# Kernel optimization log

Measured on AMD Instinct MI355X. Metric: run time of the kernel, lower is better.

Reference implementation:

```python
import jax, jax.numpy as jnp
import numpy as np

H, D, KD, E = 8, 128, 16, 128
B, G = 16, 501

def setup_inputs() -> dict:
    key = jax.random.key(0)
    ks = jax.random.split(key, 12)
    stdv = 1.0 / np.sqrt(KD)
    u = lambda k, shape, s: jax.random.uniform(k, shape, jnp.float32, -s, s)
    inp = {"q": jax.random.normal(ks[0], (B, G, D), jnp.float32)}
    names = ["W_query", "W_key", "W_val", "W1_query", "W2_query", "W3_query",
             "W4_query", "W5_query", "W6_query"]
    for i, n in enumerate(names):
        inp[n] = u(ks[i + 1], (H, D, KD), stdv)
    inp["W_out"] = u(ks[10], (H, KD, E), 1.0 / np.sqrt(E))
    return inp

def _forward(q, W_query, W_key, W_val, W1, W2, W3, W4, W5, W6, W_out):
    h = q  # self-attention: h defaults to q
    b, g, d = h.shape
    np_ = (g - 1) // 2
    norm = 1.0 / jnp.sqrt(jnp.float32(KD))
    pick = h[:, 1:np_ + 1]          # [b, np, d]
    delivery = h[:, np_ + 1:]       # [b, np, d]
    proj = lambda x, W: jnp.einsum('bnd,hdk->hbnk', x, W)
    Q = proj(q, W_query); K = proj(h, W_key); V = proj(h, W_val)
    K_pick = proj(pick, W_key); V_pick = proj(pick, W_val)
    K_del = proj(delivery, W_key); V_del = proj(delivery, W_val)
    Q_pick = proj(pick, W1); Q_pick_ap = proj(pick, W2); Q_pick_ad = proj(pick, W3)
    Q_del = proj(delivery, W4); Q_del_ad = proj(delivery, W5); Q_del_ap = proj(delivery, W6)

    comp = norm * jnp.einsum('hbqk,hbgk->hbqg', Q, K)                 # [h,b,g,g]
    c_pd = norm * jnp.sum(Q_pick * K_del, -1)                          # [h,b,np]
    c_p_ap = norm * jnp.einsum('hbqk,hbpk->hbqp', Q_pick_ap, K_pick)   # [h,b,np,np]
    c_p_ad = norm * jnp.einsum('hbqk,hbpk->hbqp', Q_pick_ad, K_del)
    c_dp = norm * jnp.sum(Q_del * K_pick, -1)                          # [h,b,np]
    c_d_ad = norm * jnp.einsum('hbqk,hbpk->hbqp', Q_del_ad, K_del)
    c_d_ap = norm * jnp.einsum('hbqk,hbpk->hbqp', Q_del_ap, K_pick)

    ninf = lambda *s: jnp.full(s, -jnp.inf, comp.dtype)
    # pad branch scores to query length g (depot row + wrong-subset rows = -inf)
    c_add_del = jnp.concatenate([ninf(H, b, 1), c_pd, ninf(H, b, np_)], -1)[..., None]            # [h,b,g,1]
    c_add_ap = jnp.concatenate([ninf(H, b, 1, np_), c_p_ap, ninf(H, b, np_, np_)], 2)             # [h,b,g,np]
    c_add_ad = jnp.concatenate([ninf(H, b, 1, np_), c_p_ad, ninf(H, b, np_, np_)], 2)
    c_add_pick = jnp.concatenate([ninf(H, b, 1), ninf(H, b, np_), c_dp], -1)[..., None]
    c_add_ad2 = jnp.concatenate([ninf(H, b, 1, np_), ninf(H, b, np_, np_), c_d_ad], 2)
    c_add_ap2 = jnp.concatenate([ninf(H, b, 1, np_), ninf(H, b, np_, np_), c_d_ap], 2)
    comp_full = jnp.concatenate([comp, c_add_del, c_add_ap, c_add_ad,
                                 c_add_pick, c_add_ad2, c_add_ap2], -1)  # [h,b,g,g+2+4*np]

    attn = jax.nn.softmax(comp_full, axis=-1)

    z = lambda *s: jnp.zeros(s, V.dtype)
    V_add_del = jnp.concatenate([z(H, b, 1, KD), V_del, z(H, b, np_, KD)], 2)   # [h,b,g,kd]
    V_add_pick = jnp.concatenate([z(H, b, 1, KD), z(H, b, np_, KD), V_pick], 2)

    mm = lambda a, v: jnp.einsum('hbqp,hbpk->hbqk', a, v)
    heads = mm(attn[..., :g], V)
    heads = heads + attn[..., g:g + 1] * V_add_del
    heads = heads + mm(attn[..., g + 1:g + 1 + np_], V_pick)
    heads = heads + mm(attn[..., g + 1 + np_:g + 1 + 2 * np_], V_del)
    heads = heads + attn[..., g + 1 + 2 * np_:g + 2 + 2 * np_] * V_add_pick
    heads = heads + mm(attn[..., g + 2 + 2 * np_:g + 2 + 3 * np_], V_del)
    heads = heads + mm(attn[..., g + 2 + 3 * np_:], V_pick)

    return jnp.einsum('hbnk,hke->bne', heads, W_out)

def reference(q, W_query, W_key, W_val, W1_query, W2_query, W3_query,
              W4_query, W5_query, W6_query, W_out):
    return _forward(q, W_query, W_key, W_val, W1_query, W2_query, W3_query,
                    W4_query, W5_query, W6_query, W_out)
```

## Files before the change

### kernel.cpp

```cpp
#include <hip/hip_runtime.h>

#define H_ 8
#define D_ 128
#define KD_ 16
#define E_ 128
#define B_ 16
#define G_ 501
#define NP_ 250
#define BN_ (B_*G_)

typedef __bf16 bf16x8 __attribute__((ext_vector_type(8)));
typedef float f32x4 __attribute__((ext_vector_type(4)));
typedef unsigned short u16x8 __attribute__((ext_vector_type(8)));
typedef unsigned short u16x4 __attribute__((ext_vector_type(4)));
typedef bf16x8 __attribute__((may_alias)) bf16x8_a;
typedef u16x8 __attribute__((may_alias)) u16x8_a;
typedef u16x4 __attribute__((may_alias)) u16x4_a;

__device__ __forceinline__ unsigned short f2bf(float f) {
  unsigned int u = __builtin_bit_cast(unsigned int, f);
  unsigned int r = u + 0x7FFFu + ((u >> 16) & 1u);
  return (unsigned short)(r >> 16);
}
__device__ __forceinline__ float bf2f(unsigned short u) {
  unsigned int v = ((unsigned int)u) << 16;
  return __builtin_bit_cast(float, v);
}

__global__ __launch_bounds__(256) void k_prep(
    const float* __restrict__ w0, const float* __restrict__ w1, const float* __restrict__ w2,
    const float* __restrict__ w3, const float* __restrict__ w4, const float* __restrict__ w5,
    const float* __restrict__ w6, const float* __restrict__ w7, const float* __restrict__ w8,
    unsigned short* __restrict__ wct) {
  int i = blockIdx.x * 256 + threadIdx.x;
  if (i < H_*9*KD_*D_) {
    int d = i & 127; int t = i >> 7; int k = t & 15; t >>= 4;
    int wi = t % 9; int h = t / 9;
    const float* src = w0;
    switch (wi) {
      case 1: src = w1; break; case 2: src = w2; break; case 3: src = w3; break;
      case 4: src = w4; break; case 5: src = w5; break; case 6: src = w6; break;
      case 7: src = w7; break; case 8: src = w8; break; default: break;
    }
    wct[i] = f2bf(src[h*(D_*KD_) + d*KD_ + k]);
  }
}

__global__ __launch_bounds__(256) void k_proj(const float* __restrict__ q,
                                              const unsigned short* __restrict__ wct,
                                              unsigned short* __restrict__ P) {
  const int tid = threadIdx.x;
  const int lane = tid & 63;
  const int wv = tid >> 6;
  const int ln = lane & 15;
  const int quad = lane >> 4;
  const int b = blockIdx.y >> 3;
  const int nt = blockIdx.y & 7;
  const int cbase = blockIdx.x * 64;

  __shared__ __align__(16) unsigned short sA[64*136];
  __shared__ __align__(16) unsigned short sB[64*136];

  for (int i = tid; i < 1024; i += 256) {
    int rr = i >> 4, half = i & 15;
    int r = min(nt*64 + rr, G_ - 1);
    const float* src = q + (size_t)(b*G_ + r)*D_ + half*8;
    float4 f0 = ((const float4*)src)[0];
    float4 f1 = ((const float4*)src)[1];
    u16x8 v;
    v[0]=f2bf(f0.x); v[1]=f2bf(f0.y); v[2]=f2bf(f0.z); v[3]=f2bf(f0.w);
    v[4]=f2bf(f1.x); v[5]=f2bf(f1.y); v[6]=f2bf(f1.z); v[7]=f2bf(f1.w);
    *(u16x8*)(sA + rr*136 + half*8) = v;
  }
  for (int i = tid; i < 1024; i += 256) {
    int cc = i >> 4, half = i & 15;
    u16x8 v = *(const u16x8*)(wct + (size_t)(cbase + cc)*D_ + half*8);
    *(u16x8*)(sB + cc*136 + half*8) = v;
  }
  __syncthreads();

  bf16x8 a[4];
  #pragma unroll
  for (int ks = 0; ks < 4; ++ks)
    a[ks] = *(const bf16x8_a*)(sA + (wv*16 + ln)*136 + ks*32 + quad*8);

  #pragma unroll
  for (int ct = 0; ct < 4; ++ct) {
    f32x4 acc = {0.f,0.f,0.f,0.f};
    #pragma unroll
    for (int ks = 0; ks < 4; ++ks) {
      bf16x8 bb = *(const bf16x8_a*)(sB + (ct*16 + ln)*136 + ks*32 + quad*8);
      acc = __builtin_amdgcn_mfma_f32_16x16x32_bf16(a[ks], bb, acc, 0,0,0);
    }
    const int c = cbase + ct*16 + ln;
    const int h = c / 144; const int rem = c - h*144; const int w = rem >> 4; const int k = rem & 15;
    const float sc = (w == 1 || w == 2) ? 1.0f : 0.25f;
    const size_t pb = ((size_t)((h*9 + w)*B_ + b)*G_)*KD_ + k;
    #pragma unroll
    for (int g = 0; g < 4; ++g) {
      const int nn = nt*64 + wv*16 + quad*4 + g;
      if (nn < G_) P[pb + (size_t)nn*KD_] = f2bf(acc[g]*sc);
    }
  }
}

__device__ __forceinline__ f32x4 mf(bf16x8 a, bf16x8 b, f32x4 c) {
  return __builtin_amdgcn_mfma_f32_16x16x32_bf16(a, b, c, 0,0,0);
}

__device__ __forceinline__ void score_chunk(
    int c, bool up, bool dn, int cbuf,
    const unsigned short* sK, bf16x8 qa, bf16x8 qp, bf16x8 qdl,
    unsigned short* eb, float rv, float& esum, int ln, int quad)
{
  const f32x4 z4 = {0.f,0.f,0.f,0.f};
  bf16x8 k0 = {}, k1 = {};
  if (quad < 2) {
    const unsigned short* kp = sK + (c*32 + ln)*16 + quad*8;
    k0 = *(const bf16x8_a*)(kp);
    k1 = *(const bf16x8_a*)(kp + 256);
  }
  f32x4 sa0 = mf(k0, qa, z4), sa1 = mf(k1, qa, z4);
  f32x4 sp0 = z4, sp1 = z4, sd0 = z4, sd1 = z4;
  if (up) { sp0 = mf(k0, qp, z4);  sp1 = mf(k1, qp, z4); }
  if (dn) { sd0 = mf(k0, qdl, z4); sd1 = mf(k1, qdl, z4); }

  float el = 0.f;
  unsigned short ev[8];
  #pragma unroll
  for (int t = 0; t < 2; ++t) {
    #pragma unroll
    for (int rg = 0; rg < 4; ++rg) {
      float comp = __expf(t ? sa1[rg] : sa0[rg]);
      if (c == 15 && t == 1) comp *= (quad*4 + rg <= 4) ? 1.f : 0.f;
      float ex = 0.f;
      if (up) {
        float m = 1.f;
        if (c == 0 && t == 0 && rg == 0) m = (quad != 0) ? 1.f : 0.f;
        if (c == 7 && t == 1) m = (quad*4 + rg <= 10) ? 1.f : 0.f;
        ex += m * __expf(t ? sp1[rg] : sp0[rg]);
      }
      if (dn) {
        float m = 1.f;
        if (c == 7)  m = (t == 1 && quad*4 + rg >= 11) ? 1.f : 0.f;
        if (c == 15 && t == 1) m = (quad*4 + rg <= 4) ? 1.f : 0.f;
        ex += m * __expf(t ? sd1[rg] : sd0[rg]);
      }
      float e = comp + rv * ex;
      el += e;
      ev[t*4 + rg] = f2bf(e);
    }
  }
  esum += el;
  u16x4 w0, w1;
  w0[0]=ev[0]; w0[1]=ev[1]; w0[2]=ev[2]; w0[3]=ev[3];
  w1[0]=ev[4]; w1[1]=ev[5]; w1[2]=ev[6]; w1[3]=ev[7];
  unsigned short* base = eb + cbuf*640 + ln*40 + quad*4;
  *(u16x4_a*)(base)      = w0;
  *(u16x4_a*)(base + 16) = w1;
}

__global__ __launch_bounds__(256, 3) void k_attn(const unsigned short* __restrict__ P,
                                                 float* __restrict__ heads) {
  const int rt = blockIdx.x, b = blockIdx.y, h = blockIdx.z;
  const int tid = threadIdx.x;
  const int lane = tid & 63;
  const int wv = tid >> 6;
  const int ln = lane & 15;
  const int quad = lane >> 4;
  const int r0 = rt * 64;

  __shared__ __align__(16) unsigned short sK [512*16];
  __shared__ __align__(16) unsigned short sVt[16*520];
  __shared__ __align__(16) unsigned short sQa[65*16];
  __shared__ __align__(16) unsigned short sQp[65*16];
  __shared__ __align__(16) unsigned short sQd[65*16];
  __shared__ __align__(16) unsigned short sQs[65*16];
  __shared__ __align__(16) unsigned short sKs[65*16];
  __shared__ __align__(16) unsigned short eBuf[4*2*640];

  const size_t slab = (size_t)G_*KD_;
  const unsigned short* Pk = P + ((size_t)(h*9+1)*B_ + b)*slab;
  const unsigned short* Pv = P + ((size_t)(h*9+2)*B_ + b)*slab;
  const u16x8 vz = {0,0,0,0,0,0,0,0};

  for (int i = tid; i < 1024; i += 256) {
    int key = i >> 1;
    u16x8 v = vz;
    if (key < G_) v = *(const u16x8*)(Pk + key*KD_ + (i & 1)*8);
    *(u16x8*)(sK + i*8) = v;
  }
  for (int i = tid; i < 8192; i += 256) {
    int key = i >> 4, kd = i & 15;
    sVt[kd*520 + key] = (key < G_) ? Pv[key*KD_ + kd] : (unsigned short)0;
  }
  for (int i = tid; i < 650; i += 256) {
    int arr = i / 130;
    int j = i - arr*130;
    int rr = j >> 1, half = j & 1;
    int r = r0 + rr;
    u16x8 v = vz;
    if (rr < 64 && r < G_) {
      bool pick = (r <= NP_);
      const unsigned short* src;
      if (arr == 4) {
        int ks = (r == 0) ? 0 : (pick ? r + NP_ : r - NP_);
        src = Pk + ks*KD_;
      } else {
        int w = (arr == 0) ? 0 : (arr == 1) ? (pick ? 4 : 8)
              : (arr == 2) ? (pick ? 5 : 7) : (pick ? 3 : 6);
        src = P + ((size_t)(h*9 + w)*B_ + b)*slab + (size_t)r*KD_;
      }
      v = *(const u16x8*)(src + half*8);
    }
    unsigned short* dst = (arr==0) ? sQa : (arr==1) ? sQp : (arr==2) ? sQd
                        : (arr==3) ? sQs : sKs;
    *(u16x8*)(dst + j*8) = v;
  }
  __syncthreads();

  const int aoff = (wv*16 + ln)*16 + quad*8;
  bf16x8 qa  = *(const bf16x8_a*)(sQa + aoff);
  bf16x8 qp  = *(const bf16x8_a*)(sQp + aoff);
  bf16x8 qdl = *(const bf16x8_a*)(sQd + aoff);

  const int rw0 = r0 + wv*16;
  const int ra = rw0 + ln;
  const float rv = (ra >= 1) ? 1.f : 0.f;
  unsigned short* eb = eBuf + wv*1280;

  f32x4 acc = {0.f,0.f,0.f,0.f};
  float esum = 0.f;

  #pragma unroll
  for (int p = 0; p < 8; ++p) {
    const int c0 = 2*p, c1 = c0 + 1;
    score_chunk(c0, c0 <= 7, c0 >= 7, 0, sK, qa, qp, qdl, eb, rv, esum, ln, quad);
    score_chunk(c1, c1 <= 7, c1 >= 7, 1, sK, qa, qp, qdl, eb, rv, esum, ln, quad);
    #pragma unroll
    for (int u = 0; u < 2; ++u) {
      bf16x8 Ef = *(const bf16x8_a*)(eb + u*640 + ln*40 + quad*8);
      bf16x8 Vf = *(const bf16x8_a*)(sVt + ln*520 + (c0+u)*32 + quad*8);
      acc = mf(Vf, Ef, acc);
    }
  }

  esum += __shfl_xor(esum, 16);
  esum += __shfl_xor(esum, 32);

  const unsigned short* qsp = sQs + (wv*16 + ln)*16;
  const unsigned short* ksp = sKs + (wv*16 + ln)*16;
  u16x8 qs0 = *(const u16x8_a*)(qsp), qs1 = *(const u16x8_a*)(qsp + 8);
  u16x8 ks0 = *(const u16x8_a*)(ksp), ks1 = *(const u16x8_a*)(ksp + 8);
  float s = 0.f;
  #pragma unroll
  for (int kd = 0; kd < 8; ++kd) {
    s = fmaf(bf2f(qs0[kd]), bf2f(ks0[kd]), s);
    s = fmaf(bf2f(qs1[kd]), bf2f(ks1[kd]), s);
  }
  const float rvs = (ra >= 1 && ra < G_) ? 1.f : 0.f;
  const float esng = rvs * __expf(s);
  esum += esng;
  const int kpair = (ra >= 1 && ra < G_) ? ((ra <= NP_) ? ra + NP_ : ra - NP_) : 0;

  const float rcp = __builtin_amdgcn_rcpf(esum);
  float4 o;
  o.x = (acc[0] + esng * bf2f(sVt[(quad*4+0)*520 + kpair])) * rcp;
  o.y = (acc[1] + esng * bf2f(sVt[(quad*4+1)*520 + kpair])) * rcp;
  o.z = (acc[2] + esng * bf2f(sVt[(quad*4+2)*520 + kpair])) * rcp;
  o.w = (acc[3] + esng * bf2f(sVt[(quad*4+3)*520 + kpair])) * rcp;
  if (ra < G_)
    *(float4*)(heads + ((size_t)(b*G_ + ra))*E_ + h*16 + quad*4) = o;
}

__global__ __launch_bounds__(256) void k_out(const float* __restrict__ heads,
                                             const float* __restrict__ wout,
                                             float* __restrict__ out) {
  const int base = blockIdx.x * 16;
  const int tid = threadIdx.x;
  __shared__ __align__(16) float sA[16*128];
  for (int i = tid; i < 512; i += 256)
    ((float4*)sA)[i] = ((const float4*)heads)[(size_t)base*32 + i];
  __syncthreads();
  const int cg = tid & 31, rh = tid >> 5;
  float4 acc0 = make_float4(0.f,0.f,0.f,0.f);
  float4 acc1 = make_float4(0.f,0.f,0.f,0.f);
  const float4* w4 = (const float4*)wout;
  #pragma unroll 8
  for (int kk = 0; kk < 128; ++kk) {
    float4 wv = w4[kk*32 + cg];
    float a0 = sA[(rh*2)*128 + kk];
    float a1 = sA[(rh*2+1)*128 + kk];
    acc0.x = fmaf(a0, wv.x, acc0.x); acc0.y = fmaf(a0, wv.y, acc0.y);
    acc0.z = fmaf(a0, wv.z, acc0.z); acc0.w = fmaf(a0, wv.w, acc0.w);
    acc1.x = fmaf(a1, wv.x, acc1.x); acc1.y = fmaf(a1, wv.y, acc1.y);
    acc1.z = fmaf(a1, wv.z, acc1.z); acc1.w = fmaf(a1, wv.w, acc1.w);
  }
  ((float4*)out)[(size_t)(base + rh*2)*32 + cg] = acc0;
  ((float4*)out)[(size_t)(base + rh*2 + 1)*32 + cg] = acc1;
}

extern "C" void kernel_launch(void* const* d_in, const int* in_sizes, int n_in,
                              void* d_out, int out_size, void* d_ws, size_t ws_size,
                              hipStream_t stream) {
  const float* q = (const float*)d_in[0];
  const float* w0 = (const float*)d_in[1];
  const float* w1 = (const float*)d_in[2];
  const float* w2 = (const float*)d_in[3];
  const float* w3 = (const float*)d_in[4];
  const float* w4 = (const float*)d_in[5];
  const float* w5 = (const float*)d_in[6];
  const float* w6 = (const float*)d_in[7];
  const float* w7 = (const float*)d_in[8];
  const float* w8 = (const float*)d_in[9];
  const float* wout = (const float*)d_in[10];
  float* out = (float*)d_out;

  char* ws = (char*)d_ws;
  unsigned short* wct = (unsigned short*)(ws);
  unsigned short* P   = (unsigned short*)(ws + 294912);
  float* heads        = (float*)(ws + 18763776);

  k_prep<<<dim3(4608), dim3(256), 0, stream>>>(w0,w1,w2,w3,w4,w5,w6,w7,w8, wct);
  k_proj<<<dim3(18, 128), dim3(256), 0, stream>>>(q, wct, P);
  k_attn<<<dim3(8, 16, 8), dim3(256), 0, stream>>>(P, heads);
  k_out<<<dim3(501), dim3(256), 0, stream>>>(heads, wout, out);
}
```

Before: 144.0 us.

## Pre-transpose V in projection, process two row tiles per attention block, MFMA output GEMM

The projection kernel now writes V directly in a transposed, padded layout, so the attention kernel can load it with vector copies instead of a scalar transpose. Each attention block handles two 64-row query tiles, reusing the shared K/V staging. The key buffer uses a padded stride, and the single-key term reads K from shared memory. Heads are stored as bf16 and the output projection switches to a bf16 MFMA GEMM; this adds rounding error and lowers occupancy to 2 blocks per CU, while halving the attention grid.

New measurement: 123.4 us. 1.17x faster.

```diff
diff --git a/kernel.cpp b/kernel.cpp
--- a/kernel.cpp
+++ b/kernel.cpp
@@ -31,7 +31,7 @@
     const float* __restrict__ w0, const float* __restrict__ w1, const float* __restrict__ w2,
     const float* __restrict__ w3, const float* __restrict__ w4, const float* __restrict__ w5,
     const float* __restrict__ w6, const float* __restrict__ w7, const float* __restrict__ w8,
-    unsigned short* __restrict__ wct) {
+    unsigned short* __restrict__ wct, unsigned short* __restrict__ Pvt) {
   int i = blockIdx.x * 256 + threadIdx.x;
   if (i < H_*9*KD_*D_) {
     int d = i & 127; int t = i >> 7; int k = t & 15; t >>= 4;
@@ -44,11 +44,16 @@
     }
     wct[i] = f2bf(src[h*(D_*KD_) + d*KD_ + k]);
   }
+  if (i < 128*16*19) {
+    int s = i / 304; int r2 = i - s*304; int k = r2 / 19; int key = 501 + (r2 - k*19);
+    Pvt[(size_t)s*8320 + k*520 + key] = 0;
+  }
 }
 
 __global__ __launch_bounds__(256) void k_proj(const float* __restrict__ q,
                                               const unsigned short* __restrict__ wct,
-                                              unsigned short* __restrict__ P) {
+                                              unsigned short* __restrict__ P,
+                                              unsigned short* __restrict__ Pvt) {
   const int tid = threadIdx.x;
   const int lane = tid & 63;
   const int wv = tid >> 6;
@@ -94,12 +99,21 @@
     }
     const int c = cbase + ct*16 + ln;
     const int h = c / 144; const int rem = c - h*144; const int w = rem >> 4; const int k = rem & 15;
-    const float sc = (w == 1 || w == 2) ? 1.0f : 0.25f;
-    const size_t pb = ((size_t)((h*9 + w)*B_ + b)*G_)*KD_ + k;
-    #pragma unroll
-    for (int g = 0; g < 4; ++g) {
-      const int nn = nt*64 + wv*16 + quad*4 + g;
-      if (nn < G_) P[pb + (size_t)nn*KD_] = f2bf(acc[g]*sc);
+    if (w == 2) {
+      unsigned short* dstv = Pvt + (size_t)(h*B_ + b)*8320 + k*520;
+      #pragma unroll
+      for (int g = 0; g < 4; ++g) {
+        const int nn = nt*64 + wv*16 + quad*4 + g;
+        if (nn < G_) dstv[nn] = f2bf(acc[g]);
+      }
+    } else {
+      const float sc = (w == 1) ? 1.0f : 0.25f;
+      const size_t pb = ((size_t)((h*9 + w)*B_ + b)*G_)*KD_ + k;
+      #pragma unroll
+      for (int g = 0; g < 4; ++g) {
+        const int nn = nt*64 + wv*16 + quad*4 + g;
+        if (nn < G_) P[pb + (size_t)nn*KD_] = f2bf(acc[g]*sc);
+      }
     }
   }
 }
@@ -116,9 +130,9 @@
   const f32x4 z4 = {0.f,0.f,0.f,0.f};
   bf16x8 k0 = {}, k1 = {};
   if (quad < 2) {
-    const unsigned short* kp = sK + (c*32 + ln)*16 + quad*8;
+    const unsigned short* kp = sK + (c*32 + ln)*24 + quad*8;
     k0 = *(const bf16x8_a*)(kp);
-    k1 = *(const bf16x8_a*)(kp + 256);
+    k1 = *(const bf16x8_a*)(kp + 384);
   }
   f32x4 sa0 = mf(k0, qa, z4), sa1 = mf(k1, qa, z4);
   f32x4 sp0 = z4, sp1 = z4, sd0 = z4, sd1 = z4;
@@ -160,144 +174,143 @@
   *(u16x4_a*)(base + 16) = w1;
 }
 
-__global__ __launch_bounds__(256, 3) void k_attn(const unsigned short* __restrict__ P,
-                                                 float* __restrict__ heads) {
-  const int rt = blockIdx.x, b = blockIdx.y, h = blockIdx.z;
+__global__ __launch_bounds__(256, 2) void k_attn(const unsigned short* __restrict__ P,
+                                                 const unsigned short* __restrict__ Pvt,
+                                                 unsigned short* __restrict__ headsb) {
+  const int rt2 = blockIdx.x, b = blockIdx.y, h = blockIdx.z;
   const int tid = threadIdx.x;
   const int lane = tid & 63;
   const int wv = tid >> 6;
   const int ln = lane & 15;
   const int quad = lane >> 4;
-  const int r0 = rt * 64;
-
-  __shared__ __align__(16) unsigned short sK [512*16];
+
+  __shared__ __align__(16) unsigned short sK [512*24];
   __shared__ __align__(16) unsigned short sVt[16*520];
-  __shared__ __align__(16) unsigned short sQa[65*16];
-  __shared__ __align__(16) unsigned short sQp[65*16];
-  __shared__ __align__(16) unsigned short sQd[65*16];
-  __shared__ __align__(16) unsigned short sQs[65*16];
-  __shared__ __align__(16) unsigned short sKs[65*16];
+  __shared__ __align__(16) unsigned short sQ [8*1040];
   __shared__ __align__(16) unsigned short eBuf[4*2*640];
 
   const size_t slab = (size_t)G_*KD_;
   const unsigned short* Pk = P + ((size_t)(h*9+1)*B_ + b)*slab;
-  const unsigned short* Pv = P + ((size_t)(h*9+2)*B_ + b)*slab;
   const u16x8 vz = {0,0,0,0,0,0,0,0};
 
   for (int i = tid; i < 1024; i += 256) {
-    int key = i >> 1;
+    int key = i >> 1, half = i & 1;
     u16x8 v = vz;
-    if (key < G_) v = *(const u16x8*)(Pk + key*KD_ + (i & 1)*8);
-    *(u16x8*)(sK + i*8) = v;
-  }
-  for (int i = tid; i < 8192; i += 256) {
-    int key = i >> 4, kd = i & 15;
-    sVt[kd*520 + key] = (key < G_) ? Pv[key*KD_ + kd] : (unsigned short)0;
-  }
-  for (int i = tid; i < 650; i += 256) {
-    int arr = i / 130;
-    int j = i - arr*130;
+    if (key < G_) v = *(const u16x8*)(Pk + key*KD_ + half*8);
+    *(u16x8*)(sK + key*24 + half*8) = v;
+  }
+  const unsigned short* pv = Pvt + (size_t)(h*B_ + b)*8320;
+  for (int i = tid; i < 1040; i += 256)
+    *(u16x8*)(sVt + i*8) = *(const u16x8*)(pv + i*8);
+  for (int i = tid; i < 1040; i += 256) {
+    int t = i / 520; int j2 = i - t*520;
+    int arr = j2 / 130; int j = j2 - arr*130;
     int rr = j >> 1, half = j & 1;
-    int r = r0 + rr;
+    int r = (rt2*2 + t)*64 + rr;
     u16x8 v = vz;
     if (rr < 64 && r < G_) {
       bool pick = (r <= NP_);
-      const unsigned short* src;
-      if (arr == 4) {
-        int ks = (r == 0) ? 0 : (pick ? r + NP_ : r - NP_);
-        src = Pk + ks*KD_;
-      } else {
-        int w = (arr == 0) ? 0 : (arr == 1) ? (pick ? 4 : 8)
-              : (arr == 2) ? (pick ? 5 : 7) : (pick ? 3 : 6);
-        src = P + ((size_t)(h*9 + w)*B_ + b)*slab + (size_t)r*KD_;
-      }
-      v = *(const u16x8*)(src + half*8);
-    }
-    unsigned short* dst = (arr==0) ? sQa : (arr==1) ? sQp : (arr==2) ? sQd
-                        : (arr==3) ? sQs : sKs;
-    *(u16x8*)(dst + j*8) = v;
+      int w = (arr==0) ? 0 : (arr==1) ? (pick?4:8) : (arr==2) ? (pick?5:7) : (pick?3:6);
+      v = *(const u16x8*)(P + ((size_t)(h*9+w)*B_ + b)*slab + (size_t)r*KD_ + half*8);
+    }
+    *(u16x8*)(sQ + (t*4+arr)*1040 + j*8) = v;
   }
   __syncthreads();
 
-  const int aoff = (wv*16 + ln)*16 + quad*8;
-  bf16x8 qa  = *(const bf16x8_a*)(sQa + aoff);
-  bf16x8 qp  = *(const bf16x8_a*)(sQp + aoff);
-  bf16x8 qdl = *(const bf16x8_a*)(sQd + aoff);
-
-  const int rw0 = r0 + wv*16;
-  const int ra = rw0 + ln;
-  const float rv = (ra >= 1) ? 1.f : 0.f;
   unsigned short* eb = eBuf + wv*1280;
 
-  f32x4 acc = {0.f,0.f,0.f,0.f};
-  float esum = 0.f;
-
-  #pragma unroll
-  for (int p = 0; p < 8; ++p) {
-    const int c0 = 2*p, c1 = c0 + 1;
-    score_chunk(c0, c0 <= 7, c0 >= 7, 0, sK, qa, qp, qdl, eb, rv, esum, ln, quad);
-    score_chunk(c1, c1 <= 7, c1 >= 7, 1, sK, qa, qp, qdl, eb, rv, esum, ln, quad);
-    #pragma unroll
-    for (int u = 0; u < 2; ++u) {
-      bf16x8 Ef = *(const bf16x8_a*)(eb + u*640 + ln*40 + quad*8);
-      bf16x8 Vf = *(const bf16x8_a*)(sVt + ln*520 + (c0+u)*32 + quad*8);
-      acc = mf(Vf, Ef, acc);
-    }
-  }
-
-  esum += __shfl_xor(esum, 16);
-  esum += __shfl_xor(esum, 32);
-
-  const unsigned short* qsp = sQs + (wv*16 + ln)*16;
-  const unsigned short* ksp = sKs + (wv*16 + ln)*16;
-  u16x8 qs0 = *(const u16x8_a*)(qsp), qs1 = *(const u16x8_a*)(qsp + 8);
-  u16x8 ks0 = *(const u16x8_a*)(ksp), ks1 = *(const u16x8_a*)(ksp + 8);
-  float s = 0.f;
-  #pragma unroll
-  for (int kd = 0; kd < 8; ++kd) {
-    s = fmaf(bf2f(qs0[kd]), bf2f(ks0[kd]), s);
-    s = fmaf(bf2f(qs1[kd]), bf2f(ks1[kd]), s);
-  }
-  const float rvs = (ra >= 1 && ra < G_) ? 1.f : 0.f;
-  const float esng = rvs * __expf(s);
-  esum += esng;
-  const int kpair = (ra >= 1 && ra < G_) ? ((ra <= NP_) ? ra + NP_ : ra - NP_) : 0;
-
-  const float rcp = __builtin_amdgcn_rcpf(esum);
-  float4 o;
-  o.x = (acc[0] + esng * bf2f(sVt[(quad*4+0)*520 + kpair])) * rcp;
-  o.y = (acc[1] + esng * bf2f(sVt[(quad*4+1)*520 + kpair])) * rcp;
-  o.z = (acc[2] + esng * bf2f(sVt[(quad*4+2)*520 + kpair])) * rcp;
-  o.w = (acc[3] + esng * bf2f(sVt[(quad*4+3)*520 + kpair])) * rcp;
-  if (ra < G_)
-    *(float4*)(heads + ((size_t)(b*G_ + ra))*E_ + h*16 + quad*4) = o;
-}
-
-__global__ __launch_bounds__(256) void k_out(const float* __restrict__ heads,
+  for (int t = 0; t < 2; ++t) {
+    const int r0 = (rt2*2 + t)*64;
+    const unsigned short* sQt = sQ + t*4160;
+    const int aoff = (wv*16 + ln)*16 + quad*8;
+    bf16x8 qa  = *(const bf16x8_a*)(sQt + aoff);
+    bf16x8 qp  = *(const bf16x8_a*)(sQt + 1040 + aoff);
+    bf16x8 qdl = *(const bf16x8_a*)(sQt + 2080 + aoff);
+
+    const int ra = r0 + wv*16 + ln;
+    const float rv = (ra >= 1) ? 1.f : 0.f;
+
+    f32x4 acc = {0.f,0.f,0.f,0.f};
+    float esum = 0.f;
+
+    #pragma unroll
+    for (int p = 0; p < 8; ++p) {
+      const int c0 = 2*p, c1 = c0 + 1;
+      score_chunk(c0, c0 <= 7, c0 >= 7, 0, sK, qa, qp, qdl, eb, rv, esum, ln, quad);
+      score_chunk(c1, c1 <= 7, c1 >= 7, 1, sK, qa, qp, qdl, eb, rv, esum, ln, quad);
+      #pragma unroll
+      for (int u = 0; u < 2; ++u) {
+        bf16x8 Ef = *(const bf16x8_a*)(eb + u*640 + ln*40 + quad*8);
+        bf16x8 Vf = *(const bf16x8_a*)(sVt + ln*520 + (c0+u)*32 + quad*8);
+        acc = mf(Vf, Ef, acc);
+      }
+    }
+
+    esum += __shfl_xor(esum, 16);
+    esum += __shfl_xor(esum, 32);
+
+    const unsigned short* qsp = sQt + 3120 + (wv*16 + ln)*16;
+    const int kpair = (ra >= 1 && ra < G_) ? ((ra <= NP_) ? ra + NP_ : ra - NP_) : 0;
+    const unsigned short* ksp = sK + kpair*24;
+    u16x8 qs0 = *(const u16x8_a*)(qsp), qs1 = *(const u16x8_a*)(qsp + 8);
+    u16x8 ks0 = *(const u16x8_a*)(ksp), ks1 = *(const u16x8_a*)(ksp + 8);
+    float s = 0.f;
+    #pragma unroll
+    for (int kd = 0; kd < 8; ++kd) {
+      s = fmaf(bf2f(qs0[kd]), bf2f(ks0[kd]), s);
+      s = fmaf(bf2f(qs1[kd]), bf2f(ks1[kd]), s);
+    }
+    const float rvs = (ra >= 1 && ra < G_) ? 1.f : 0.f;
+    const float esng = rvs * __expf(s);
+    const float rcp = __builtin_amdgcn_rcpf(esum + esng);
+
+    u16x4 ov;
+    ov[0] = f2bf((acc[0] + esng * bf2f(sVt[(quad*4+0)*520 + kpair])) * rcp);
+    ov[1] = f2bf((acc[1] + esng * bf2f(sVt[(quad*4+1)*520 + kpair])) * rcp);
+    ov[2] = f2bf((acc[2] + esng * bf2f(sVt[(quad*4+2)*520 + kpair])) * rcp);
+    ov[3] = f2bf((acc[3] + esng * bf2f(sVt[(quad*4+3)*520 + kpair])) * rcp);
+    if (ra < G_)
+      *(u16x4*)(headsb + ((size_t)(b*G_ + ra))*E_ + h*16 + quad*4) = ov;
+  }
+}
+
+__global__ __launch_bounds__(256) void k_out(const unsigned short* __restrict__ headsb,
                                              const float* __restrict__ wout,
                                              float* __restrict__ out) {
-  const int base = blockIdx.x * 16;
   const int tid = threadIdx.x;
-  __shared__ __align__(16) float sA[16*128];
-  for (int i = tid; i < 512; i += 256)
-    ((float4*)sA)[i] = ((const float4*)heads)[(size_t)base*32 + i];
+  const int lane = tid & 63;
+  const int wv = tid >> 6;
+  const int ln = lane & 15;
+  const int quad = lane >> 4;
+  const int base = blockIdx.x * 64;
+
+  __shared__ __align__(16) unsigned short sWt[128*136];
+  for (int i = tid; i < 16384; i += 256) {
+    int k = i >> 7, e = i & 127;
+    sWt[e*136 + k] = f2bf(wout[i]);
+  }
   __syncthreads();
-  const int cg = tid & 31, rh = tid >> 5;
-  float4 acc0 = make_float4(0.f,0.f,0.f,0.f);
-  float4 acc1 = make_float4(0.f,0.f,0.f,0.f);
-  const float4* w4 = (const float4*)wout;
-  #pragma unroll 8
-  for (int kk = 0; kk < 128; ++kk) {
-    float4 wv = w4[kk*32 + cg];
-    float a0 = sA[(rh*2)*128 + kk];
-    float a1 = sA[(rh*2+1)*128 + kk];
-    acc0.x = fmaf(a0, wv.x, acc0.x); acc0.y = fmaf(a0, wv.y, acc0.y);
-    acc0.z = fmaf(a0, wv.z, acc0.z); acc0.w = fmaf(a0, wv.w, acc0.w);
-    acc1.x = fmaf(a1, wv.x, acc1.x); acc1.y = fmaf(a1, wv.y, acc1.y);
-    acc1.z = fmaf(a1, wv.z, acc1.z); acc1.w = fmaf(a1, wv.w, acc1.w);
-  }
-  ((float4*)out)[(size_t)(base + rh*2)*32 + cg] = acc0;
-  ((float4*)out)[(size_t)(base + rh*2 + 1)*32 + cg] = acc1;
+
+  const int row = min(base + wv*16 + ln, BN_ - 1);
+  bf16x8 a[4];
+  #pragma unroll
+  for (int ks = 0; ks < 4; ++ks)
+    a[ks] = *(const bf16x8_a*)(headsb + (size_t)row*E_ + ks*32 + quad*8);
+
+  #pragma unroll
+  for (int ct = 0; ct < 8; ++ct) {
+    f32x4 acc = {0.f,0.f,0.f,0.f};
+    #pragma unroll
+    for (int ks = 0; ks < 4; ++ks) {
+      bf16x8 bb = *(const bf16x8_a*)(sWt + (ct*16 + ln)*136 + ks*32 + quad*8);
+      acc = __builtin_amdgcn_mfma_f32_16x16x32_bf16(a[ks], bb, acc, 0,0,0);
+    }
+    #pragma unroll
+    for (int g = 0; g < 4; ++g) {
+      const int r = base + wv*16 + quad*4 + g;
+      if (r < BN_) out[(size_t)r*E_ + ct*16 + ln] = acc[g];
+    }
+  }
 }
 
 extern "C" void kernel_launch(void* const* d_in, const int* in_sizes, int n_in,
@@ -317,12 +330,13 @@
   float* out = (float*)d_out;
 
   char* ws = (char*)d_ws;
-  unsigned short* wct = (unsigned short*)(ws);
-  unsigned short* P   = (unsigned short*)(ws + 294912);
-  float* heads        = (float*)(ws + 18763776);
-
-  k_prep<<<dim3(4608), dim3(256), 0, stream>>>(w0,w1,w2,w3,w4,w5,w6,w7,w8, wct);
-  k_proj<<<dim3(18, 128), dim3(256), 0, stream>>>(q, wct, P);
-  k_attn<<<dim3(8, 16, 8), dim3(256), 0, stream>>>(P, heads);
-  k_out<<<dim3(501), dim3(256), 0, stream>>>(heads, wout, out);
-}
+  unsigned short* wct    = (unsigned short*)(ws);
+  unsigned short* P      = (unsigned short*)(ws + 294912);
+  unsigned short* Pvt    = (unsigned short*)(ws + 18763776);
+  unsigned short* headsb = (unsigned short*)(ws + 20893696);
+
+  k_prep<<<dim3(576), dim3(256), 0, stream>>>(w0,w1,w2,w3,w4,w5,w6,w7,w8, wct, Pvt);
+  k_proj<<<dim3(18, 128), dim3(256), 0, stream>>>(q, wct, P, Pvt);
+  k_attn<<<dim3(4, 16, 8), dim3(256), 0, stream>>>(P, Pvt, headsb);
+  k_out<<<dim3(126), dim3(256), 0, stream>>>(headsb, wout, out);
+}
```
